# Kernel optimization log

Measured on AMD Instinct MI355X. Metric: run time of the kernel, lower is better.

## Reference

```python
import jax, jax.numpy as jnp
import numpy as np


def setup_inputs() -> dict:
    key = jax.random.key(0)
    ks = jax.random.split(key, 6)
    B, C, W, H = 8, 512, 64, 64
    return {
        "x": jax.random.normal(ks[0], (B, C, W, H), dtype=jnp.float32),
        "proj_query": jax.random.normal(ks[1], (C, W, H), dtype=jnp.float32),
        "key_w": jax.random.normal(ks[2], (C, C), dtype=jnp.float32) * 0.02,
        "key_b": jax.random.normal(ks[3], (C,), dtype=jnp.float32) * 0.02,
        "value_w": jax.random.normal(ks[4], (C, C), dtype=jnp.float32) * 0.02,
        "value_b": jax.random.normal(ks[5], (C,), dtype=jnp.float32) * 0.02,
        "gamma": jnp.ones((1,), dtype=jnp.float32),
    }


def reference(x, proj_query, key_w, key_b, value_w, value_b, gamma):
    B, C, W, H = x.shape
    N = W * H
    # fixed memory query: (C, N); torch builds B x N x C via permute
    q = proj_query.reshape(C, N)
    # 1x1 convs == per-pixel channel matmuls
    k = jnp.einsum('oc,bchw->bohw', key_w, x) + key_b[None, :, None, None]
    v = jnp.einsum('oc,bchw->bohw', value_w, x) + value_b[None, :, None, None]
    k = k.reshape(B, C, N)
    v = v.reshape(B, C, N)
    # energy = bmm(key [B,C,N], query^T [N,C]) -> B x C x C (channel attention)
    energy = jnp.einsum('bcn,dn->bcd', k, q)
    attention = jax.nn.softmax(energy, axis=-1)
    # out = bmm(attention^T [B,C,C], value [B,C,N]) -> B x C x N
    out = jnp.einsum('bdc,bdn->bcn', attention, v)
    out = out.reshape(B, C, W, H)
    return gamma * out + x
```

## Files before the change

### kernel.cpp

```cpp
#include <hip/hip_runtime.h>

typedef unsigned short u16;
typedef unsigned int u32;
typedef unsigned long long u64;
typedef _Float16 f16x8 __attribute__((ext_vector_type(8)));
typedef float f32x4 __attribute__((ext_vector_type(4)));

__device__ __forceinline__ u16 f2h(float f) {
  union { _Float16 h; u16 u; } c; c.h = (_Float16)f; return c.u;
}
__device__ __forceinline__ float h2f(u16 v) {
  union { u16 u; _Float16 h; } c; c.u = v; return (float)c.h;
}

__device__ __forceinline__ f32x4 mfma16(f16x8 a, f16x8 b, f32x4 c) {
  return __builtin_amdgcn_mfma_f32_16x16x32_f16(a, b, c, 0, 0, 0);
}

__device__ __forceinline__ void ld8f(const float* s, u16* o) {
  float4 a = *(const float4*)s;
  float4 b = *(const float4*)(s + 4);
  o[0] = f2h(a.x); o[1] = f2h(a.y); o[2] = f2h(a.z); o[3] = f2h(a.w);
  o[4] = f2h(b.x); o[5] = f2h(b.y); o[6] = f2h(b.z); o[7] = f2h(b.w);
}

__device__ __forceinline__ void glds16(const u16* g, u16* l) {
  __builtin_amdgcn_global_load_lds(
      reinterpret_cast<const __attribute__((address_space(1))) u32*>(reinterpret_cast<u64>(g)),
      reinterpret_cast<__attribute__((address_space(3))) u32*>(reinterpret_cast<u64>(l)),
      16, 0, 0);
}

template<int TM, int TN>
__device__ __forceinline__ void gemm_core(const u16* __restrict__ A, int lda,
                                          const u16* __restrict__ B, int ldb,
                                          int ksteps, u16* sA, u16* sB, f32x4 acc[TM][TN]) {
  const int t = threadIdx.x;
  const int lane = t & 63, wave = t >> 6;
  const int wm = wave >> 1, wn = wave & 1;
  const int m16 = lane & 15, q4 = lane >> 4;
  constexpr int BM = TM * 32, BN = TN * 32;
  constexpr int TILEA = BM * 32, TILEB = BN * 32;
  constexpr int APF = BM / 64, BPF = BN / 64;
  constexpr int VPI = APF + BPF;

  int aoff[APF], asl[APF];
#pragma unroll
  for (int p = 0; p < APF; ++p) {
    int s = p * 256 + t, row = s >> 2;
    int kc = (s & 3) ^ ((row >> 1) & 3);
    aoff[p] = row * lda + kc * 8;
    asl[p] = (p * 256 + (t & 192)) * 8;
  }
  int boff[BPF], bsl[BPF];
#pragma unroll
  for (int p = 0; p < BPF; ++p) {
    int s = p * 256 + t, row = s >> 2;
    int kc = (s & 3) ^ ((row >> 1) & 3);
    boff[p] = row * ldb + kc * 8;
    bsl[p] = (p * 256 + (t & 192)) * 8;
  }

  int aro[TM], bro[TN];
#pragma unroll
  for (int i = 0; i < TM; ++i) {
    int row = wm * TM * 16 + i * 16 + m16;
    aro[i] = row * 32 + ((q4 ^ ((row >> 1) & 3)) << 3);
  }
#pragma unroll
  for (int j = 0; j < TN; ++j) {
    int row = wn * TN * 16 + j * 16 + m16;
    bro[j] = row * 32 + ((q4 ^ ((row >> 1) & 3)) << 3);
  }

  u16 *aR = sA, *aS = sA + TILEA, *aT = sA + 2 * TILEA;
  u16 *bR = sB, *bS = sB + TILEB, *bT = sB + 2 * TILEB;

#pragma unroll
  for (int p = 0; p < APF; ++p) glds16(A + aoff[p], aR + asl[p]);
#pragma unroll
  for (int p = 0; p < BPF; ++p) glds16(B + boff[p], bR + bsl[p]);

#pragma unroll 1
  for (int kt = 0; kt < ksteps; ++kt) {
    const bool more = kt + 1 < ksteps;

    if (more) {
      const u16* An = A + (kt + 1) * 32;
#pragma unroll
      for (int p = 0; p < APF; ++p) glds16(An + aoff[p], aS + asl[p]);
      const u16* Bn = B + (kt + 1) * 32;
#pragma unroll
      for (int p = 0; p < BPF; ++p) glds16(Bn + boff[p], bS + bsl[p]);
      asm volatile("s_waitcnt vmcnt(%0)" :: "n"(VPI) : "memory");
    } else {
      asm volatile("s_waitcnt vmcnt(0)" ::: "memory");
    }
    __builtin_amdgcn_s_barrier();
    __builtin_amdgcn_sched_barrier(0);

    f16x8 af[TM], bv[TN];
#pragma unroll
    for (int i = 0; i < TM; ++i) af[i] = *(const f16x8*)&aR[aro[i]];
#pragma unroll
    for (int j = 0; j < TN; ++j) bv[j] = *(const f16x8*)&bR[bro[j]];
#pragma unroll
    for (int i = 0; i < TM; ++i)
#pragma unroll
      for (int j = 0; j < TN; ++j)
        acc[i][j] = mfma16(af[i], bv[j], acc[i][j]);

    { u16* x = aR; aR = aS; aS = aT; aT = x; }
    { u16* x = bR; bR = bS; bS = bT; bT = x; }
  }
}

__global__ __launch_bounds__(256) void cvt_xt_kernel(const float* __restrict__ x,
                                                     u16* __restrict__ xh,
                                                     u16* __restrict__ xhT) {
  __shared__ __align__(16) u16 T[64 * 72];
  int nt = blockIdx.x, ot = blockIdx.y, b = blockIdx.z;
  int t = threadIdx.x;
  int s = t & 31;
  int c = (t >> 5) * 8;

  const float* xp = x + ((size_t)b * 512 + ot * 64 + 2 * s) * 4096 + nt * 64 + c;
  u16 r0[8], r1[8];
  ld8f(xp, r0);
  ld8f(xp + 4096, r1);

  u16* xq = xh + ((size_t)b * 512 + ot * 64 + 2 * s) * 4096 + nt * 64 + c;
  *(int4*)xq = *(int4*)r0;
  *(int4*)(xq + 4096) = *(int4*)r1;

  u32* Tw = (u32*)T;
#pragma unroll
  for (int e = 0; e < 8; ++e)
    Tw[(c + e) * 36 + s] = (u32)r0[e] | ((u32)r1[e] << 16);
  __syncthreads();

  int rr = t >> 2, og = t & 3;
  int4 v0 = *(const int4*)&T[rr * 72 + og * 16];
  int4 v1 = *(const int4*)&T[rr * 72 + og * 16 + 8];
  u16* xo = xhT + ((size_t)b * 4096 + nt * 64 + rr) * 512 + ot * 64 + og * 16;
  *(int4*)xo = v0;
  *(int4*)(xo + 8) = v1;
}

__global__ __launch_bounds__(256) void cvt_q_kernel(const float* __restrict__ q, u16* __restrict__ qh,
                                                    float* __restrict__ qs) {
  int row = blockIdx.x, t = threadIdx.x;
  float s = 0.f;
#pragma unroll
  for (int p = 0; p < 2; ++p) {
    size_t i = (size_t)row * 4096 + p * 2048 + t * 8;
    u16 o[8];
    ld8f(q + i, o);
#pragma unroll
    for (int e = 0; e < 8; ++e) s += h2f(o[e]);
    *(int4*)&qh[i] = *(int4*)o;
  }
  for (int off = 32; off; off >>= 1) s += __shfl_xor(s, off);
  __shared__ float wsum[4];
  if ((t & 63) == 0) wsum[t >> 6] = s;
  __syncthreads();
  if (t == 0) qs[row] = wsum[0] + wsum[1] + wsum[2] + wsum[3];
}

__global__ __launch_bounds__(256) void prep_kernel(const float* __restrict__ vw, u16* __restrict__ vwT,
                                                   const float* __restrict__ kw, u16* __restrict__ kwh,
                                                   float* __restrict__ beta) {
  int blk = blockIdx.x, t = threadIdx.x;
  if (blk < 256) {
    __shared__ u16 sT[32 * 33];
    int bx = blk & 15, by = blk >> 4;
#pragma unroll
    for (int p = 0; p < 4; ++p) {
      int idx = p * 256 + t; int r = idx >> 5, c = idx & 31;
      sT[r * 33 + c] = f2h(vw[(size_t)(by * 32 + r) * 512 + bx * 32 + c]);
    }
    __syncthreads();
#pragma unroll
    for (int p = 0; p < 4; ++p) {
      int idx = p * 256 + t; int r = idx >> 5, c = idx & 31;
      vwT[(size_t)(bx * 32 + r) * 512 + by * 32 + c] = sT[c * 33 + r];
    }
  } else if (blk < 384) {
    size_t i = ((size_t)(blk - 256) * 256 + t) * 8;
    u16 o[8];
    ld8f(kw + i, o);
    *(int4*)&kwh[i] = *(int4*)o;
  } else {
    for (int i = t; i < 4096; i += 256) beta[i] = 0.f;
  }
}

__global__ __launch_bounds__(256) void sgemm_kernel(const u16* __restrict__ qh, const u16* __restrict__ xh,
                                                    u16* __restrict__ Sh) {
  __shared__ __align__(16) u16 sA[3 * 64 * 32], sB[3 * 64 * 32];
  int rt = blockIdx.x, jt = blockIdx.y;
  f32x4 acc[2][2];
#pragma unroll
  for (int i = 0; i < 2; ++i)
#pragma unroll
    for (int j = 0; j < 2; ++j) acc[i][j] = (f32x4){0.f, 0.f, 0.f, 0.f};
  gemm_core<2, 2>(qh + (size_t)jt * 64 * 4096, 4096,
                  xh + (size_t)rt * 64 * 4096, 4096, 128, sA, sB, acc);

  const int t = threadIdx.x, lane = t & 63, wave = t >> 6;
  const int wm = wave >> 1, wn = wave & 1, m16 = lane & 15, q4 = lane >> 4;
  int b = (rt * 64) >> 9, o0 = (rt * 64) & 511;
  u16* Ob = Sh + (size_t)b * 262144;
#pragma unroll
  for (int i = 0; i < 2; ++i)
#pragma unroll
    for (int j = 0; j < 2; ++j)
#pragma unroll
      for (int r = 0; r < 4; ++r) {
        int y = jt * 64 + wm * 32 + i * 16 + q4 * 4 + r;
        int o = o0 + wn * 32 + j * 16 + m16;
        Ob[(size_t)y * 512 + o] = f2h(acc[i][j][r]);
      }
}

__global__ __launch_bounds__(256) void egemm_kernel(const u16* __restrict__ kwh, const u16* __restrict__ Sh,
                                                    float* __restrict__ E) {
  __shared__ __align__(16) u16 sA[3 * 64 * 32], sB[3 * 64 * 32];
  int xt = blockIdx.x >> 3, yt = blockIdx.x & 7, b = blockIdx.y;
  f32x4 acc[2][2];
#pragma unroll
  for (int i = 0; i < 2; ++i)
#pragma unroll
    for (int j = 0; j < 2; ++j) acc[i][j] = (f32x4){0.f, 0.f, 0.f, 0.f};
  gemm_core<2, 2>(kwh + (size_t)xt * 64 * 512, 512,
                  Sh + (size_t)b * 262144 + (size_t)yt * 64 * 512, 512, 16, sA, sB, acc);

  const int t = threadIdx.x, lane = t & 63, wave = t >> 6;
  const int wm = wave >> 1, wn = wave & 1, m16 = lane & 15, q4 = lane >> 4;
  float* O = E + ((size_t)b * 512 + xt * 64) * 512 + yt * 64;
#pragma unroll
  for (int i = 0; i < 2; ++i)
#pragma unroll
    for (int j = 0; j < 2; ++j)
#pragma unroll
      for (int r = 0; r < 4; ++r) {
        int row = wm * 32 + i * 16 + q4 * 4 + r;
        int col = wn * 32 + j * 16 + m16;
        O[(size_t)row * 512 + col] = acc[i][j][r];
      }
}

__global__ __launch_bounds__(256) void softmax_kernel(const float* __restrict__ E, const float* __restrict__ qs,
                                                      const float* __restrict__ kb, const float* __restrict__ vb,
                                                      u16* __restrict__ attT, float* __restrict__ beta) {
  __shared__ float sE[16 * 516];
  __shared__ float sM[16], sS[16];
  int i0 = blockIdx.x * 16, b = blockIdx.y, t = threadIdx.x;
  const float* Eb = E + ((size_t)b * 512 + i0) * 512;
  for (int ch = 0; ch < 32; ++ch) {
    int idx = ch * 256 + t;
    int row = idx >> 9, col = idx & 511;
    sE[row * 516 + col] = Eb[(size_t)row * 512 + col] + kb[i0 + row] * qs[col];
  }
  __syncthreads();
  {
    int row = t >> 4, sub = t & 15;
    float mx = -1e30f;
    for (int ii = 0; ii < 32; ++ii) mx = fmaxf(mx, sE[row * 516 + sub + ii * 16]);
    for (int off = 8; off; off >>= 1) mx = fmaxf(mx, __shfl_xor(mx, off));
    float sm = 0.f;
    for (int ii = 0; ii < 32; ++ii) sm += __expf(sE[row * 516 + sub + ii * 16] - mx);
    for (int off = 8; off; off >>= 1) sm += __shfl_xor(sm, off);
    if (sub == 0) { sM[row] = mx; sS[row] = 1.f / sm; }
  }
  __syncthreads();
  float vbr = vb[i0 + (t & 15)];
  u16* Ob = attT + (size_t)b * 262144;
  for (int ch = 0; ch < 32; ++ch) {
    int idx = ch * 256 + t;
    int r = idx & 15, j = idx >> 4;
    float a = __expf(sE[r * 516 + j] - sM[r]) * sS[r];
    Ob[(size_t)j * 512 + i0 + r] = f2h(a);
    float part = a * vbr;
    for (int off = 8; off; off >>= 1) part += __shfl_xor(part, off);
    if (r == 0) atomicAdd(&beta[b * 512 + j], part);
  }
}

__global__ __launch_bounds__(256) void wgemm_kernel(const u16* __restrict__ attT, const u16* __restrict__ vwT,
                                                    u16* __restrict__ W) {
  __shared__ __align__(16) u16 sA[3 * 64 * 32], sB[3 * 64 * 32];
  int ct = blockIdx.x >> 3, ot = blockIdx.x & 7, b = blockIdx.y;
  f32x4 acc[2][2];
#pragma unroll
  for (int i = 0; i < 2; ++i)
#pragma unroll
    for (int j = 0; j < 2; ++j) acc[i][j] = (f32x4){0.f, 0.f, 0.f, 0.f};
  gemm_core<2, 2>(attT + (size_t)b * 262144 + (size_t)ct * 64 * 512, 512,
                  vwT + (size_t)ot * 64 * 512, 512, 16, sA, sB, acc);

  const int t = threadIdx.x, lane = t & 63, wave = t >> 6;
  const int wm = wave >> 1, wn = wave & 1, m16 = lane & 15, q4 = lane >> 4;
  u16* O = W + (size_t)b * 262144 + (size_t)(ct * 64) * 512 + ot * 64;
#pragma unroll
  for (int i = 0; i < 2; ++i)
#pragma unroll
    for (int j = 0; j < 2; ++j)
#pragma unroll
      for (int r = 0; r < 4; ++r) {
        int row = wm * 32 + i * 16 + q4 * 4 + r;
        int col = wn * 32 + j * 16 + m16;
        O[(size_t)row * 512 + col] = f2h(acc[i][j][r]);
      }
}

__global__ __launch_bounds__(256) void outgemm_kernel(const u16* __restrict__ W, const u16* __restrict__ xhT,
                                                      const float* __restrict__ x, const float* __restrict__ beta,
                                                      const float* __restrict__ gm, float* __restrict__ out) {
  __shared__ __align__(16) u16 sA[3 * 128 * 32], sB[3 * 128 * 32];
  int nt = blockIdx.x, ct = blockIdx.y, b = blockIdx.z;
  f32x4 acc[4][4];
#pragma unroll
  for (int i = 0; i < 4; ++i)
#pragma unroll
    for (int j = 0; j < 4; ++j) acc[i][j] = (f32x4){0.f, 0.f, 0.f, 0.f};
  gemm_core<4, 4>(W + (size_t)b * 262144 + (size_t)ct * 128 * 512, 512,
                  xhT + (size_t)b * 2097152 + (size_t)nt * 128 * 512, 512, 16, sA, sB, acc);

  const int t = threadIdx.x, lane = t & 63, wave = t >> 6;
  const int wm = wave >> 1, wn = wave & 1, m16 = lane & 15, q4 = lane >> 4;
  float g = gm[0];
#pragma unroll
  for (int i = 0; i < 4; ++i)
#pragma unroll
    for (int j = 0; j < 4; ++j)
#pragma unroll
      for (int r = 0; r < 4; ++r) {
        int c = ct * 128 + wm * 64 + i * 16 + q4 * 4 + r;
        int n = nt * 128 + wn * 64 + j * 16 + m16;
        size_t idx = (size_t)b * 2097152 + (size_t)c * 4096 + n;
        out[idx] = g * (acc[i][j][r] + beta[b * 512 + c]) + x[idx];
      }
}

extern "C" void kernel_launch(void* const* d_in, const int* in_sizes, int n_in,
                              void* d_out, int out_size, void* d_ws, size_t ws_size,
                              hipStream_t stream) {
  const float* x  = (const float*)d_in[0];
  const float* pq = (const float*)d_in[1];
  const float* kw = (const float*)d_in[2];
  const float* kb = (const float*)d_in[3];
  const float* vw = (const float*)d_in[4];
  const float* vb = (const float*)d_in[5];
  const float* gm = (const float*)d_in[6];
  float* out = (float*)d_out;

  char* ws = (char*)d_ws;
  u16*   xh   = (u16*)(ws);
  u16*   qh   = (u16*)(ws + (32ull << 20));
  u16*   Sh   = (u16*)(ws + (36ull << 20));
  u16*   W    = (u16*)(ws + (36ull << 20));
  float* E    = (float*)(ws + (40ull << 20));
  u16*   attT = (u16*)(ws + (48ull << 20));
  u16*   kwh  = (u16*)(ws + (52ull << 20));
  u16*   vwT  = (u16*)(ws + (52ull << 20) + 524288);
  char*  sm   = ws + (53ull << 20);
  float* qs   = (float*)(sm);
  float* beta = (float*)(sm + 4096);
  u16*   xhT  = (u16*)(ws + (54ull << 20));

  cvt_xt_kernel<<<dim3(64, 8, 8), 256, 0, stream>>>(x, xh, xhT);
  cvt_q_kernel<<<dim3(512), 256, 0, stream>>>(pq, qh, qs);
  prep_kernel<<<dim3(385), 256, 0, stream>>>(vw, vwT, kw, kwh, beta);
  sgemm_kernel<<<dim3(64, 8), 256, 0, stream>>>(qh, xh, Sh);
  egemm_kernel<<<dim3(64, 8), 256, 0, stream>>>(kwh, Sh, E);
  softmax_kernel<<<dim3(32, 8), 256, 0, stream>>>(E, qs, kb, vb, attT, beta);
  wgemm_kernel<<<dim3(64, 8), 256, 0, stream>>>(attT, vwT, W);
  outgemm_kernel<<<dim3(32, 4, 8), 256, 0, stream>>>(W, xhT, x, beta, gm, out);
}
```

Baseline: 246.3 us.

## Deepen GEMM prefetch, merge prep kernels, widen output GEMM tile

The shared GEMM core gains a configurable wave layout and pipeline depth. The 64x64 GEMMs now use four LDS stages with two tiles prefetched ahead, to hide more global-load latency. The three preprocessing kernels are merged into one launch to cut launch gaps and tail effects. The output GEMM moves to 512-thread blocks with a 128x256 tile, which reuses each W tile across twice as many columns but halves the grid and raises register and LDS pressure.

```diff
diff --git a/kernel.cpp b/kernel.cpp
--- a/kernel.cpp
+++ b/kernel.cpp
@@ -31,34 +31,39 @@
       16, 0, 0);
 }
 
-template<int TM, int TN>
+template<int TM, int TN, int WM, int WN, int DEPTH>
 __device__ __forceinline__ void gemm_core(const u16* __restrict__ A, int lda,
                                           const u16* __restrict__ B, int ldb,
                                           int ksteps, u16* sA, u16* sB, f32x4 acc[TM][TN]) {
+  constexpr int NT = WM * WN * 64;
+  constexpr int BM = WM * TM * 16, BN = WN * TN * 16;
+  constexpr int TILEA = BM * 32, TILEB = BN * 32;
+  constexpr int APF = (BM * 4) / NT, BPF = (BN * 4) / NT;
+  constexpr int VPI = APF + BPF;
+  constexpr int PF = DEPTH - 2;
+  static_assert(PF == 1 || PF == 2, "");
+  static_assert(APF >= 1 && BPF >= 1, "");
+
   const int t = threadIdx.x;
   const int lane = t & 63, wave = t >> 6;
-  const int wm = wave >> 1, wn = wave & 1;
+  const int wm = wave / WN, wn = wave % WN;
   const int m16 = lane & 15, q4 = lane >> 4;
-  constexpr int BM = TM * 32, BN = TN * 32;
-  constexpr int TILEA = BM * 32, TILEB = BN * 32;
-  constexpr int APF = BM / 64, BPF = BN / 64;
-  constexpr int VPI = APF + BPF;
 
   int aoff[APF], asl[APF];
 #pragma unroll
   for (int p = 0; p < APF; ++p) {
-    int s = p * 256 + t, row = s >> 2;
+    int s = p * NT + t, row = s >> 2;
     int kc = (s & 3) ^ ((row >> 1) & 3);
     aoff[p] = row * lda + kc * 8;
-    asl[p] = (p * 256 + (t & 192)) * 8;
+    asl[p] = (p * NT + (wave << 6)) * 8;
   }
   int boff[BPF], bsl[BPF];
 #pragma unroll
   for (int p = 0; p < BPF; ++p) {
-    int s = p * 256 + t, row = s >> 2;
+    int s = p * NT + t, row = s >> 2;
     int kc = (s & 3) ^ ((row >> 1) & 3);
     boff[p] = row * ldb + kc * 8;
-    bsl[p] = (p * 256 + (t & 192)) * 8;
+    bsl[p] = (p * NT + (wave << 6)) * 8;
   }
 
   int aro[TM], bro[TN];
@@ -73,32 +78,42 @@
     bro[j] = row * 32 + ((q4 ^ ((row >> 1) & 3)) << 3);
   }
 
-  u16 *aR = sA, *aS = sA + TILEA, *aT = sA + 2 * TILEA;
-  u16 *bR = sB, *bS = sB + TILEB, *bT = sB + 2 * TILEB;
-
-#pragma unroll
-  for (int p = 0; p < APF; ++p) glds16(A + aoff[p], aR + asl[p]);
-#pragma unroll
-  for (int p = 0; p < BPF; ++p) glds16(B + boff[p], bR + bsl[p]);
-
+#pragma unroll
+  for (int j = 0; j < PF; ++j) {
+    const u16* Aj = A + j * 32;
+    u16* aS = sA + j * TILEA;
+#pragma unroll
+    for (int p = 0; p < APF; ++p) glds16(Aj + aoff[p], aS + asl[p]);
+    const u16* Bj = B + j * 32;
+    u16* bS = sB + j * TILEB;
+#pragma unroll
+    for (int p = 0; p < BPF; ++p) glds16(Bj + boff[p], bS + bsl[p]);
+  }
+
+  int cur = 0, stg = PF;
 #pragma unroll 1
   for (int kt = 0; kt < ksteps; ++kt) {
-    const bool more = kt + 1 < ksteps;
-
-    if (more) {
-      const u16* An = A + (kt + 1) * 32;
+    if (kt + PF < ksteps) {
+      const u16* An = A + (size_t)(kt + PF) * 32;
+      u16* aS = sA + stg * TILEA;
 #pragma unroll
       for (int p = 0; p < APF; ++p) glds16(An + aoff[p], aS + asl[p]);
-      const u16* Bn = B + (kt + 1) * 32;
+      const u16* Bn = B + (size_t)(kt + PF) * 32;
+      u16* bS = sB + stg * TILEB;
 #pragma unroll
       for (int p = 0; p < BPF; ++p) glds16(Bn + boff[p], bS + bsl[p]);
+    }
+    if (PF == 2 && kt + 2 < ksteps)
+      asm volatile("s_waitcnt vmcnt(%0)" :: "n"(2 * VPI) : "memory");
+    else if (kt + 1 < ksteps)
       asm volatile("s_waitcnt vmcnt(%0)" :: "n"(VPI) : "memory");
-    } else {
+    else
       asm volatile("s_waitcnt vmcnt(0)" ::: "memory");
-    }
     __builtin_amdgcn_s_barrier();
     __builtin_amdgcn_sched_barrier(0);
 
+    const u16* aR = sA + cur * TILEA;
+    const u16* bR = sB + cur * TILEB;
     f16x8 af[TM], bv[TN];
 #pragma unroll
     for (int i = 0; i < TM; ++i) af[i] = *(const f16x8*)&aR[aro[i]];
@@ -110,70 +125,67 @@
       for (int j = 0; j < TN; ++j)
         acc[i][j] = mfma16(af[i], bv[j], acc[i][j]);
 
-    { u16* x = aR; aR = aS; aS = aT; aT = x; }
-    { u16* x = bR; bR = bS; bS = bT; bT = x; }
-  }
-}
-
-__global__ __launch_bounds__(256) void cvt_xt_kernel(const float* __restrict__ x,
-                                                     u16* __restrict__ xh,
-                                                     u16* __restrict__ xhT) {
+    cur = (cur + 1 == DEPTH) ? 0 : cur + 1;
+    stg = (stg + 1 == DEPTH) ? 0 : stg + 1;
+  }
+}
+
+__global__ __launch_bounds__(256) void prep_all_kernel(const float* __restrict__ x,
+                                                       u16* __restrict__ xh, u16* __restrict__ xhT,
+                                                       const float* __restrict__ q, u16* __restrict__ qh,
+                                                       float* __restrict__ qs,
+                                                       const float* __restrict__ vw, u16* __restrict__ vwT,
+                                                       const float* __restrict__ kw, u16* __restrict__ kwh,
+                                                       float* __restrict__ beta) {
   __shared__ __align__(16) u16 T[64 * 72];
-  int nt = blockIdx.x, ot = blockIdx.y, b = blockIdx.z;
-  int t = threadIdx.x;
-  int s = t & 31;
-  int c = (t >> 5) * 8;
-
-  const float* xp = x + ((size_t)b * 512 + ot * 64 + 2 * s) * 4096 + nt * 64 + c;
-  u16 r0[8], r1[8];
-  ld8f(xp, r0);
-  ld8f(xp + 4096, r1);
-
-  u16* xq = xh + ((size_t)b * 512 + ot * 64 + 2 * s) * 4096 + nt * 64 + c;
-  *(int4*)xq = *(int4*)r0;
-  *(int4*)(xq + 4096) = *(int4*)r1;
-
-  u32* Tw = (u32*)T;
-#pragma unroll
-  for (int e = 0; e < 8; ++e)
-    Tw[(c + e) * 36 + s] = (u32)r0[e] | ((u32)r1[e] << 16);
-  __syncthreads();
-
-  int rr = t >> 2, og = t & 3;
-  int4 v0 = *(const int4*)&T[rr * 72 + og * 16];
-  int4 v1 = *(const int4*)&T[rr * 72 + og * 16 + 8];
-  u16* xo = xhT + ((size_t)b * 4096 + nt * 64 + rr) * 512 + ot * 64 + og * 16;
-  *(int4*)xo = v0;
-  *(int4*)(xo + 8) = v1;
-}
-
-__global__ __launch_bounds__(256) void cvt_q_kernel(const float* __restrict__ q, u16* __restrict__ qh,
-                                                    float* __restrict__ qs) {
-  int row = blockIdx.x, t = threadIdx.x;
-  float s = 0.f;
-#pragma unroll
-  for (int p = 0; p < 2; ++p) {
-    size_t i = (size_t)row * 4096 + p * 2048 + t * 8;
-    u16 o[8];
-    ld8f(q + i, o);
-#pragma unroll
-    for (int e = 0; e < 8; ++e) s += h2f(o[e]);
-    *(int4*)&qh[i] = *(int4*)o;
-  }
-  for (int off = 32; off; off >>= 1) s += __shfl_xor(s, off);
-  __shared__ float wsum[4];
-  if ((t & 63) == 0) wsum[t >> 6] = s;
-  __syncthreads();
-  if (t == 0) qs[row] = wsum[0] + wsum[1] + wsum[2] + wsum[3];
-}
-
-__global__ __launch_bounds__(256) void prep_kernel(const float* __restrict__ vw, u16* __restrict__ vwT,
-                                                   const float* __restrict__ kw, u16* __restrict__ kwh,
-                                                   float* __restrict__ beta) {
   int blk = blockIdx.x, t = threadIdx.x;
-  if (blk < 256) {
-    __shared__ u16 sT[32 * 33];
-    int bx = blk & 15, by = blk >> 4;
+  if (blk < 4096) {
+    int nt = blk & 63, ot = (blk >> 6) & 7, b = blk >> 9;
+    int s = t & 31;
+    int c = (t >> 5) * 8;
+
+    const float* xp = x + ((size_t)b * 512 + ot * 64 + 2 * s) * 4096 + nt * 64 + c;
+    u16 r0[8], r1[8];
+    ld8f(xp, r0);
+    ld8f(xp + 4096, r1);
+
+    u16* xq = xh + ((size_t)b * 512 + ot * 64 + 2 * s) * 4096 + nt * 64 + c;
+    *(int4*)xq = *(int4*)r0;
+    *(int4*)(xq + 4096) = *(int4*)r1;
+
+    u32* Tw = (u32*)T;
+#pragma unroll
+    for (int e = 0; e < 8; ++e)
+      Tw[(c + e) * 36 + s] = (u32)r0[e] | ((u32)r1[e] << 16);
+    __syncthreads();
+
+    int rr = t >> 2, og = t & 3;
+    int4 v0 = *(const int4*)&T[rr * 72 + og * 16];
+    int4 v1 = *(const int4*)&T[rr * 72 + og * 16 + 8];
+    u16* xo = xhT + ((size_t)b * 4096 + nt * 64 + rr) * 512 + ot * 64 + og * 16;
+    *(int4*)xo = v0;
+    *(int4*)(xo + 8) = v1;
+  } else if (blk < 4608) {
+    int row = blk - 4096;
+    float s = 0.f;
+#pragma unroll
+    for (int p = 0; p < 2; ++p) {
+      size_t i = (size_t)row * 4096 + p * 2048 + t * 8;
+      u16 o[8];
+      ld8f(q + i, o);
+#pragma unroll
+      for (int e = 0; e < 8; ++e) s += h2f(o[e]);
+      *(int4*)&qh[i] = *(int4*)o;
+    }
+    for (int off = 32; off; off >>= 1) s += __shfl_xor(s, off);
+    __shared__ float wsum[4];
+    if ((t & 63) == 0) wsum[t >> 6] = s;
+    __syncthreads();
+    if (t == 0) qs[row] = wsum[0] + wsum[1] + wsum[2] + wsum[3];
+  } else if (blk < 4864) {
+    int bi = blk - 4608;
+    u16* sT = T;
+    int bx = bi & 15, by = bi >> 4;
 #pragma unroll
     for (int p = 0; p < 4; ++p) {
       int idx = p * 256 + t; int r = idx >> 5, c = idx & 31;
@@ -185,8 +197,8 @@
       int idx = p * 256 + t; int r = idx >> 5, c = idx & 31;
       vwT[(size_t)(bx * 32 + r) * 512 + by * 32 + c] = sT[c * 33 + r];
     }
-  } else if (blk < 384) {
-    size_t i = ((size_t)(blk - 256) * 256 + t) * 8;
+  } else if (blk < 4992) {
+    size_t i = ((size_t)(blk - 4864) * 256 + t) * 8;
     u16 o[8];
     ld8f(kw + i, o);
     *(int4*)&kwh[i] = *(int4*)o;
@@ -197,15 +209,15 @@
 
 __global__ __launch_bounds__(256) void sgemm_kernel(const u16* __restrict__ qh, const u16* __restrict__ xh,
                                                     u16* __restrict__ Sh) {
-  __shared__ __align__(16) u16 sA[3 * 64 * 32], sB[3 * 64 * 32];
+  __shared__ __align__(16) u16 sA[4 * 64 * 32], sB[4 * 64 * 32];
   int rt = blockIdx.x, jt = blockIdx.y;
   f32x4 acc[2][2];
 #pragma unroll
   for (int i = 0; i < 2; ++i)
 #pragma unroll
     for (int j = 0; j < 2; ++j) acc[i][j] = (f32x4){0.f, 0.f, 0.f, 0.f};
-  gemm_core<2, 2>(qh + (size_t)jt * 64 * 4096, 4096,
-                  xh + (size_t)rt * 64 * 4096, 4096, 128, sA, sB, acc);
+  gemm_core<2, 2, 2, 2, 4>(qh + (size_t)jt * 64 * 4096, 4096,
+                           xh + (size_t)rt * 64 * 4096, 4096, 128, sA, sB, acc);
 
   const int t = threadIdx.x, lane = t & 63, wave = t >> 6;
   const int wm = wave >> 1, wn = wave & 1, m16 = lane & 15, q4 = lane >> 4;
@@ -225,15 +237,15 @@
 
 __global__ __launch_bounds__(256) void egemm_kernel(const u16* __restrict__ kwh, const u16* __restrict__ Sh,
                                                     float* __restrict__ E) {
-  __shared__ __align__(16) u16 sA[3 * 64 * 32], sB[3 * 64 * 32];
+  __shared__ __align__(16) u16 sA[4 * 64 * 32], sB[4 * 64 * 32];
   int xt = blockIdx.x >> 3, yt = blockIdx.x & 7, b = blockIdx.y;
   f32x4 acc[2][2];
 #pragma unroll
   for (int i = 0; i < 2; ++i)
 #pragma unroll
     for (int j = 0; j < 2; ++j) acc[i][j] = (f32x4){0.f, 0.f, 0.f, 0.f};
-  gemm_core<2, 2>(kwh + (size_t)xt * 64 * 512, 512,
-                  Sh + (size_t)b * 262144 + (size_t)yt * 64 * 512, 512, 16, sA, sB, acc);
+  gemm_core<2, 2, 2, 2, 4>(kwh + (size_t)xt * 64 * 512, 512,
+                           Sh + (size_t)b * 262144 + (size_t)yt * 64 * 512, 512, 16, sA, sB, acc);
 
   const int t = threadIdx.x, lane = t & 63, wave = t >> 6;
   const int wm = wave >> 1, wn = wave & 1, m16 = lane & 15, q4 = lane >> 4;
@@ -289,15 +301,15 @@
 
 __global__ __launch_bounds__(256) void wgemm_kernel(const u16* __restrict__ attT, const u16* __restrict__ vwT,
                                                     u16* __restrict__ W) {
-  __shared__ __align__(16) u16 sA[3 * 64 * 32], sB[3 * 64 * 32];
+  __shared__ __align__(16) u16 sA[4 * 64 * 32], sB[4 * 64 * 32];
   int ct = blockIdx.x >> 3, ot = blockIdx.x & 7, b = blockIdx.y;
   f32x4 acc[2][2];
 #pragma unroll
   for (int i = 0; i < 2; ++i)
 #pragma unroll
     for (int j = 0; j < 2; ++j) acc[i][j] = (f32x4){0.f, 0.f, 0.f, 0.f};
-  gemm_core<2, 2>(attT + (size_t)b * 262144 + (size_t)ct * 64 * 512, 512,
-                  vwT + (size_t)ot * 64 * 512, 512, 16, sA, sB, acc);
+  gemm_core<2, 2, 2, 2, 4>(attT + (size_t)b * 262144 + (size_t)ct * 64 * 512, 512,
+                           vwT + (size_t)ot * 64 * 512, 512, 16, sA, sB, acc);
 
   const int t = threadIdx.x, lane = t & 63, wave = t >> 6;
   const int wm = wave >> 1, wn = wave & 1, m16 = lane & 15, q4 = lane >> 4;
@@ -314,21 +326,21 @@
       }
 }
 
-__global__ __launch_bounds__(256) void outgemm_kernel(const u16* __restrict__ W, const u16* __restrict__ xhT,
-                                                      const float* __restrict__ x, const float* __restrict__ beta,
-                                                      const float* __restrict__ gm, float* __restrict__ out) {
-  __shared__ __align__(16) u16 sA[3 * 128 * 32], sB[3 * 128 * 32];
+__global__ __launch_bounds__(512, 4) void outgemm_kernel(const u16* __restrict__ W, const u16* __restrict__ xhT,
+                                                         const float* __restrict__ x, const float* __restrict__ beta,
+                                                         const float* __restrict__ gm, float* __restrict__ out) {
+  __shared__ __align__(16) u16 sA[3 * 128 * 32], sB[3 * 256 * 32];
   int nt = blockIdx.x, ct = blockIdx.y, b = blockIdx.z;
   f32x4 acc[4][4];
 #pragma unroll
   for (int i = 0; i < 4; ++i)
 #pragma unroll
     for (int j = 0; j < 4; ++j) acc[i][j] = (f32x4){0.f, 0.f, 0.f, 0.f};
-  gemm_core<4, 4>(W + (size_t)b * 262144 + (size_t)ct * 128 * 512, 512,
-                  xhT + (size_t)b * 2097152 + (size_t)nt * 128 * 512, 512, 16, sA, sB, acc);
+  gemm_core<4, 4, 2, 4, 3>(W + (size_t)b * 262144 + (size_t)ct * 128 * 512, 512,
+                           xhT + (size_t)b * 2097152 + (size_t)nt * 256 * 512, 512, 16, sA, sB, acc);
 
   const int t = threadIdx.x, lane = t & 63, wave = t >> 6;
-  const int wm = wave >> 1, wn = wave & 1, m16 = lane & 15, q4 = lane >> 4;
+  const int wm = wave >> 2, wn = wave & 3, m16 = lane & 15, q4 = lane >> 4;
   float g = gm[0];
 #pragma unroll
   for (int i = 0; i < 4; ++i)
@@ -337,7 +349,7 @@
 #pragma unroll
       for (int r = 0; r < 4; ++r) {
         int c = ct * 128 + wm * 64 + i * 16 + q4 * 4 + r;
-        int n = nt * 128 + wn * 64 + j * 16 + m16;
+        int n = nt * 256 + wn * 64 + j * 16 + m16;
         size_t idx = (size_t)b * 2097152 + (size_t)c * 4096 + n;
         out[idx] = g * (acc[i][j][r] + beta[b * 512 + c]) + x[idx];
       }
@@ -369,12 +381,10 @@
   float* beta = (float*)(sm + 4096);
   u16*   xhT  = (u16*)(ws + (54ull << 20));
 
-  cvt_xt_kernel<<<dim3(64, 8, 8), 256, 0, stream>>>(x, xh, xhT);
-  cvt_q_kernel<<<dim3(512), 256, 0, stream>>>(pq, qh, qs);
-  prep_kernel<<<dim3(385), 256, 0, stream>>>(vw, vwT, kw, kwh, beta);
+  prep_all_kernel<<<dim3(4993), 256, 0, stream>>>(x, xh, xhT, pq, qh, qs, vw, vwT, kw, kwh, beta);
   sgemm_kernel<<<dim3(64, 8), 256, 0, stream>>>(qh, xh, Sh);
   egemm_kernel<<<dim3(64, 8), 256, 0, stream>>>(kwh, Sh, E);
   softmax_kernel<<<dim3(32, 8), 256, 0, stream>>>(E, qs, kb, vb, attT, beta);
   wgemm_kernel<<<dim3(64, 8), 256, 0, stream>>>(attT, vwT, W);
-  outgemm_kernel<<<dim3(32, 4, 8), 256, 0, stream>>>(W, xhT, x, beta, gm, out);
-}
+  outgemm_kernel<<<dim3(16, 4, 8), 512, 0, stream>>>(W, xhT, x, beta, gm, out);
+}
```

Measured after the change: 241.4 us. No clear change (-2.0%).
